# Kernel optimization log

Hardware: AMD Instinct MI355X
Metric: run time of the kernel (lower is better)

## Reference

```python
import jax, jax.numpy as jnp
import numpy as np

G = 256      # num graphs
M = 256      # max nodes per graph
N = G * M    # total nodes
E = N * 16   # total edges
C = 3        # num_class
K = 5        # prototypes per class
D = 128      # embedding_dim
MAXLEN = 3   # max_length


def setup_inputs() -> dict:
    key = jax.random.key(0)
    ks = jax.random.split(key, 8)
    hg = jax.random.normal(ks[0], (G, D), jnp.float32)
    H_init = jax.random.normal(ks[1], (C, K, D), jnp.float32)
    path_weight = jnp.ones((MAXLEN,), jnp.float32) * 0.5
    # per-class edge attention in (0,1), strictly interior for infoloss logs
    sij = jax.random.uniform(ks[2], (C, E), jnp.float32) * 0.98 + 0.01
    # edges constrained within each graph (batch is block-contiguous)
    src = jax.random.randint(ks[3], (E,), 0, N)
    dst = (src // M) * M + jax.random.randint(ks[4], (E,), 0, M)
    edge_index = jnp.stack([src, dst]).astype(jnp.int32)
    batch = (jnp.arange(N) // M).astype(jnp.int32)
    s = jax.random.randint(ks[5], (G,), 0, M).astype(jnp.int32)
    t = jax.random.randint(ks[6], (G,), 0, M).astype(jnp.int32)
    return dict(hg=hg, H_init=H_init, path_weight=path_weight, sij=sij,
                edge_index=edge_index, batch=batch, s=s, t=t)


def check_zero(x):
    return jnp.where(x == 0, x + 1e-8, x)


def to_dense_adj(edge_index, batch, vals):
    # scatter edge vals into [G, M, M] dense per-graph adjacency
    src, dst = edge_index[0], edge_index[1]
    g = batch[src]
    r = src - g * M
    c = dst - g * M
    return jnp.zeros((G, M, M), vals.dtype).at[g, r, c].add(vals)


def infoloss(att):
    r = 0.5
    return (att * jnp.log(att / r + 1e-6)
            + (1 - att) * jnp.log((1 - att) / (1 - r + 1e-6) + 1e-6)).mean()


def path_loss3(Mdj, Adj, s, t, weight):
    gid = jnp.arange(G)
    u = Mdj[gid, s, :]            # [G, M]
    mk = Mdj[gid, :, t]           # [G, M]
    a = Adj[gid, s, :]
    ak = Adj[gid, :, t]
    uk = Mdj[gid, s, t] / check_zero(Adj[gid, s, t])
    for l in range(MAXLEN - 1):
        tmp = (u * mk) / check_zero(a * ak)
        w = jnp.power(tmp.max(axis=1) + 1e-8, jnp.float32(1.0 / (l + 1)))
        uk = uk + weight[l + 1] * w
        # power iteration: u <- u @ Mdj, a <- a @ Adj (batched over graphs)
        u = jnp.einsum('gm,gmn->gn', u, Mdj)
        a = jnp.einsum('gm,gmn->gn', a, Adj)
    uk = uk / MAXLEN
    return -jnp.mean(jnp.log(uk + 1e-8))


def reference(hg, H_init, path_weight, sij, edge_index, batch, s, t):
    # binary dense adjacency (detached in original)
    Adj = jax.lax.stop_gradient(
        to_dense_adj(edge_index, batch, jnp.ones((E,), jnp.float32)))
    weight = jnp.clip(path_weight, 1e-10, 1.0)

    def per_class(Hc, sij_c):
        # per-class prototype attention
        scores = hg @ Hc.T                     # [G, K]
        att = jax.nn.softmax(scores, axis=-1)
        H_emb = att @ Hc                       # [G, D]
        # dense weighted adjacency from per-class edge attention
        Mdj = to_dense_adj(edge_index, batch, sij_c)
        L_path = path_loss3(Mdj, Adj, s, t, weight)
        L_l2 = (jnp.sum(sij_c ** 2) / 2) / G
        L_info = infoloss(sij_c)
        return H_emb, L_info, L_path, L_l2

    H_out, L_info, L_path, L_l2 = jax.vmap(per_class)(H_init, sij)
    return (H_out, L_info.mean(), L_path.mean(), L_l2.mean())
```

## Files before the change

### kernel.cpp

```cpp
#include <hip/hip_runtime.h>
#include <math.h>

#define G 256
#define M 256
#define NNODES (G*M)
#define EDGES (NNODES*16)
#define C 3
#define K 5
#define D 128
#define GM (G*M)

#define OFF_U0   0
#define OFF_MK0  196608
#define OFF_U1   393216
#define OFF_A0   589824
#define OFF_AK0  655360
#define OFF_A1   720896
#define OFF_MST  786432
#define OFF_AST  787200
#define ZERO_FLOATS 787456
#define NB_EDGE  512
#define NB_EMB   384
#define OFF_PINFO 787456
#define OFF_PL2   (OFF_PINFO + NB_EDGE)
#define OFF_PPATH (OFF_PL2 + NB_EDGE)
#define WS_FLOATS (OFF_PPATH + C*G)

__device__ __forceinline__ float waveReduceSum(float v) {
    #pragma unroll
    for (int o = 32; o > 0; o >>= 1) v += __shfl_xor(v, o, 64);
    return v;
}
__device__ __forceinline__ float waveReduceMax(float v) {
    #pragma unroll
    for (int o = 32; o > 0; o >>= 1) v = fmaxf(v, __shfl_xor(v, o, 64));
    return v;
}

__global__ void passA(const float* __restrict__ sij, const int* __restrict__ ei,
                      const int* __restrict__ s, const int* __restrict__ t,
                      const float* __restrict__ hg, const float* __restrict__ Hm,
                      float* __restrict__ out, float* __restrict__ ws) {
    __shared__ int   sS[G], sT[G];
    __shared__ float sc[2][K];
    __shared__ float att[2][K];
    __shared__ float sInfo[4], sL2[4];

    if (blockIdx.x >= NB_EDGE) {
        int half = threadIdx.x >> 7;
        int d = threadIdx.x & 127;
        int pair = (blockIdx.x - NB_EDGE) * 2 + half;
        int c = pair / G, g = pair - c * G;
        float h = hg[g * D + d];
        if (d < K) sc[half][d] = 0.f;
        __syncthreads();
        #pragma unroll
        for (int k = 0; k < K; ++k) {
            float p = h * Hm[(c * K + k) * D + d];
            p = waveReduceSum(p);
            if ((threadIdx.x & 63) == 0) atomicAdd(&sc[half][k], p);
        }
        __syncthreads();
        if (d == 0) {
            float m = sc[half][0];
            #pragma unroll
            for (int k = 1; k < K; ++k) m = fmaxf(m, sc[half][k]);
            float sum = 0.f, ex[K];
            #pragma unroll
            for (int k = 0; k < K; ++k) { ex[k] = __expf(sc[half][k] - m); sum += ex[k]; }
            #pragma unroll
            for (int k = 0; k < K; ++k) att[half][k] = ex[k] / sum;
        }
        __syncthreads();
        float o = 0.f;
        #pragma unroll
        for (int k = 0; k < K; ++k) o += att[half][k] * Hm[(c * K + k) * D + d];
        out[pair * D + d] = o;
        return;
    }

    sS[threadIdx.x] = s[threadIdx.x];
    sT[threadIdx.x] = t[threadIdx.x];
    __syncthreads();

    float* u0  = ws + OFF_U0;
    float* mk0 = ws + OFF_MK0;
    float* a0  = ws + OFF_A0;
    float* ak0 = ws + OFF_AK0;
    float* Mst = ws + OFF_MST;
    float* Ast = ws + OFF_AST;

    int tid = blockIdx.x * 256 + threadIdx.x;
    int e0 = tid * 8;
    int4 srcA = *(const int4*)(ei + e0);
    int4 srcB = *(const int4*)(ei + e0 + 4);
    int4 dstA = *(const int4*)(ei + EDGES + e0);
    int4 dstB = *(const int4*)(ei + EDGES + e0 + 4);
    float4 v0a = *(const float4*)(sij + 0 * EDGES + e0);
    float4 v0b = *(const float4*)(sij + 0 * EDGES + e0 + 4);
    float4 v1a = *(const float4*)(sij + 1 * EDGES + e0);
    float4 v1b = *(const float4*)(sij + 1 * EDGES + e0 + 4);
    float4 v2a = *(const float4*)(sij + 2 * EDGES + e0);
    float4 v2b = *(const float4*)(sij + 2 * EDGES + e0 + 4);

    int srcp[8], dstp[8];
    float vp[3][8];
    *(int4*)&srcp[0] = srcA;  *(int4*)&srcp[4] = srcB;
    *(int4*)&dstp[0] = dstA;  *(int4*)&dstp[4] = dstB;
    *(float4*)&vp[0][0] = v0a; *(float4*)&vp[0][4] = v0b;
    *(float4*)&vp[1][0] = v1a; *(float4*)&vp[1][4] = v1b;
    *(float4*)&vp[2][0] = v2a; *(float4*)&vp[2][4] = v2b;

    float info = 0.f, l2 = 0.f;
    #pragma unroll
    for (int j = 0; j < 8; ++j) {
        int src = srcp[j], dst = dstp[j];
        int g = src >> 8;
        int r = src & 255;
        int c = dst - (g << 8);
        float v[C] = { vp[0][j], vp[1][j], vp[2][j] };
        if (r == sS[g]) {
            #pragma unroll
            for (int cc = 0; cc < C; ++cc) atomicAdd(&u0[cc * GM + (g << 8) + c], v[cc]);
            atomicAdd(&a0[(g << 8) + c], 1.0f);
            if (c == sT[g]) {
                #pragma unroll
                for (int cc = 0; cc < C; ++cc) atomicAdd(&Mst[cc * G + g], v[cc]);
                atomicAdd(&Ast[g], 1.0f);
            }
        }
        if (c == sT[g]) {
            #pragma unroll
            for (int cc = 0; cc < C; ++cc) atomicAdd(&mk0[cc * GM + (g << 8) + r], v[cc]);
            atomicAdd(&ak0[(g << 8) + r], 1.0f);
        }
        #pragma unroll
        for (int cc = 0; cc < C; ++cc) {
            float x = v[cc];
            info += x * __logf(x * 2.0f + 1e-6f)
                  + (1.0f - x) * __logf((1.0f - x) / 0.500001f + 1e-6f);
            l2 += x * x;
        }
    }
    info = waveReduceSum(info);
    l2 = waveReduceSum(l2);
    int wid = threadIdx.x >> 6, lane = threadIdx.x & 63;
    if (lane == 0) { sInfo[wid] = info; sL2[wid] = l2; }
    __syncthreads();
    if (threadIdx.x == 0) {
        float i2 = 0.f, l = 0.f;
        #pragma unroll
        for (int w = 0; w < 4; ++w) { i2 += sInfo[w]; l += sL2[w]; }
        ws[OFF_PINFO + blockIdx.x] = i2;
        ws[OFF_PL2 + blockIdx.x] = l;
    }
}

__global__ void passB(const float* __restrict__ sij, const int* __restrict__ ei,
                      float* __restrict__ ws) {
    const float* u0 = ws + OFF_U0;
    const float* a0 = ws + OFF_A0;
    float* u1 = ws + OFF_U1;
    float* a1 = ws + OFF_A1;

    int tid = blockIdx.x * 256 + threadIdx.x;
    int e0 = tid * 8;
    int4 srcA = *(const int4*)(ei + e0);
    int4 srcB = *(const int4*)(ei + e0 + 4);
    int4 dstA = *(const int4*)(ei + EDGES + e0);
    int4 dstB = *(const int4*)(ei + EDGES + e0 + 4);
    int srcp[8], dstp[8];
    *(int4*)&srcp[0] = srcA;  *(int4*)&srcp[4] = srcB;
    *(int4*)&dstp[0] = dstA;  *(int4*)&dstp[4] = dstB;

    #pragma unroll
    for (int j = 0; j < 8; ++j) {
        int src = srcp[j], dst = dstp[j];
        int g = src >> 8;
        int r = src & 255;
        int c = dst - (g << 8);
        float ar = a0[(g << 8) + r];
        if (ar == 0.0f) continue;
        atomicAdd(&a1[(g << 8) + c], ar);
        int e = e0 + j;
        #pragma unroll
        for (int cc = 0; cc < C; ++cc) {
            float ur = u0[cc * GM + (g << 8) + r];
            atomicAdd(&u1[cc * GM + (g << 8) + c], ur * sij[cc * EDGES + e]);
        }
    }
}

__global__ void pathK(const float* __restrict__ pw, float* __restrict__ ws) {
    int b = blockIdx.x;
    int c = b / G, g = b - c * G;
    int x = threadIdx.x;
    const float* u0  = ws + OFF_U0;
    const float* mk0 = ws + OFF_MK0;
    const float* u1  = ws + OFF_U1;
    const float* a0  = ws + OFF_A0;
    const float* ak0 = ws + OFF_AK0;
    const float* a1  = ws + OFF_A1;

    int gi  = (g << 8) + x;
    int cgi = c * GM + gi;
    float ak = ak0[gi], mk = mk0[cgi];
    float den0 = a0[gi] * ak;  den0 = (den0 == 0.f) ? 1e-8f : den0;
    float t0 = u0[cgi] * mk / den0;
    float den1 = a1[gi] * ak;  den1 = (den1 == 0.f) ? 1e-8f : den1;
    float t1 = u1[cgi] * mk / den1;

    t0 = waveReduceMax(t0);
    t1 = waveReduceMax(t1);
    __shared__ float s0[4], s1[4];
    int wid = x >> 6, lane = x & 63;
    if (lane == 0) { s0[wid] = t0; s1[wid] = t1; }
    __syncthreads();
    if (x == 0) {
        float m0 = s0[0], m1 = s1[0];
        #pragma unroll
        for (int w = 1; w < 4; ++w) { m0 = fmaxf(m0, s0[w]); m1 = fmaxf(m1, s1[w]); }
        float w1 = fminf(fmaxf(pw[1], 1e-10f), 1.0f);
        float w2 = fminf(fmaxf(pw[2], 1e-10f), 1.0f);
        float A = ws[OFF_AST + g];  A = (A == 0.f) ? 1e-8f : A;
        float uk = ws[OFF_MST + c * G + g] / A;
        uk += w1 * (m0 + 1e-8f);
        uk += w2 * sqrtf(m1 + 1e-8f);
        uk *= (1.0f / 3.0f);
        ws[OFF_PPATH + b] = __logf(uk + 1e-8f);
    }
}

__global__ void finalK(const float* __restrict__ ws, float* __restrict__ out) {
    int tid = threadIdx.x;
    float info = 0.f, l2 = 0.f, path = 0.f;
    for (int i = tid; i < NB_EDGE; i += 256) {
        info += ws[OFF_PINFO + i];
        l2   += ws[OFF_PL2 + i];
    }
    for (int i = tid; i < C * G; i += 256) path += ws[OFF_PPATH + i];
    info = waveReduceSum(info);
    l2   = waveReduceSum(l2);
    path = waveReduceSum(path);
    __shared__ float sI[4], sL[4], sP[4];
    int wid = tid >> 6, lane = tid & 63;
    if (lane == 0) { sI[wid] = info; sL[wid] = l2; sP[wid] = path; }
    __syncthreads();
    if (tid == 0) {
        float i2 = 0.f, l = 0.f, p = 0.f;
        #pragma unroll
        for (int w = 0; w < 4; ++w) { i2 += sI[w]; l += sL[w]; p += sP[w]; }
        out[C * G * D + 0] = i2 / (float)(C * EDGES);
        out[C * G * D + 1] = -p / (float)(C * G);
        out[C * G * D + 2] = l / (2.0f * (float)G * (float)C);
    }
}

extern "C" void kernel_launch(void* const* d_in, const int* in_sizes, int n_in,
                              void* d_out, int out_size, void* d_ws, size_t ws_size,
                              hipStream_t stream) {
    const float* hg  = (const float*)d_in[0];
    const float* Hm  = (const float*)d_in[1];
    const float* pw  = (const float*)d_in[2];
    const float* sij = (const float*)d_in[3];
    const int*   ei  = (const int*)d_in[4];
    const int*   s   = (const int*)d_in[6];
    const int*   t   = (const int*)d_in[7];
    float* out = (float*)d_out;
    float* ws  = (float*)d_ws;

    hipMemsetAsync(d_ws, 0, ZERO_FLOATS * sizeof(float), stream);
    passA<<<NB_EDGE + NB_EMB, 256, 0, stream>>>(sij, ei, s, t, hg, Hm, out, ws);
    passB<<<NB_EDGE, 256, 0, stream>>>(sij, ei, ws);
    pathK<<<C * G, M, 0, stream>>>(pw, ws);
    finalK<<<1, 256, 0, stream>>>(ws, out);
}
```

Measured before the change: 42.05 us.

## Replace memset with zeroing kernel, fuse final reduction into path kernel

Replaces the hipMemsetAsync with a custom zeroing kernel that also runs the prototype-embedding work, moving that work out of passA. The final reduction is folded into the path kernel: a global atomic counter lets the last block sum the partials. passB also hoists the a0 gathers into a separate loop so the loads can be issued together. This trims launch count and serial tail latency, at the cost of threadfence/atomic overhead in every path block.

```diff
diff --git a/kernel.cpp b/kernel.cpp
--- a/kernel.cpp
+++ b/kernel.cpp
@@ -18,10 +18,12 @@
 #define OFF_A1   720896
 #define OFF_MST  786432
 #define OFF_AST  787200
-#define ZERO_FLOATS 787456
+#define OFF_CNT  787456
+#define ZERO_FLOATS 787472
 #define NB_EDGE  512
+#define NB_ZERO  512
 #define NB_EMB   384
-#define OFF_PINFO 787456
+#define OFF_PINFO 787472
 #define OFF_PL2   (OFF_PINFO + NB_EDGE)
 #define OFF_PPATH (OFF_PL2 + NB_EDGE)
 #define WS_FLOATS (OFF_PPATH + C*G)
@@ -37,47 +39,57 @@
     return v;
 }
 
+__global__ void zeroEmb(const float* __restrict__ hg, const float* __restrict__ Hm,
+                        float* __restrict__ out, float* __restrict__ ws) {
+    __shared__ float sc[2][K];
+    __shared__ float att[2][K];
+
+    if (blockIdx.x < NB_ZERO) {
+        int tid = blockIdx.x * 256 + threadIdx.x;
+        #pragma unroll
+        for (int it = 0; it < 2; ++it) {
+            int idx = (tid + it * NB_ZERO * 256) * 4;
+            if (idx < ZERO_FLOATS)
+                *(float4*)(ws + idx) = make_float4(0.f, 0.f, 0.f, 0.f);
+        }
+        return;
+    }
+    int half = threadIdx.x >> 7;
+    int d = threadIdx.x & 127;
+    int pair = (blockIdx.x - NB_ZERO) * 2 + half;
+    int c = pair / G, g = pair - c * G;
+    float h = hg[g * D + d];
+    if (d < K) sc[half][d] = 0.f;
+    __syncthreads();
+    #pragma unroll
+    for (int k = 0; k < K; ++k) {
+        float p = h * Hm[(c * K + k) * D + d];
+        p = waveReduceSum(p);
+        if ((threadIdx.x & 63) == 0) atomicAdd(&sc[half][k], p);
+    }
+    __syncthreads();
+    if (d == 0) {
+        float m = sc[half][0];
+        #pragma unroll
+        for (int k = 1; k < K; ++k) m = fmaxf(m, sc[half][k]);
+        float sum = 0.f, ex[K];
+        #pragma unroll
+        for (int k = 0; k < K; ++k) { ex[k] = __expf(sc[half][k] - m); sum += ex[k]; }
+        #pragma unroll
+        for (int k = 0; k < K; ++k) att[half][k] = ex[k] / sum;
+    }
+    __syncthreads();
+    float o = 0.f;
+    #pragma unroll
+    for (int k = 0; k < K; ++k) o += att[half][k] * Hm[(c * K + k) * D + d];
+    out[pair * D + d] = o;
+}
+
 __global__ void passA(const float* __restrict__ sij, const int* __restrict__ ei,
                       const int* __restrict__ s, const int* __restrict__ t,
-                      const float* __restrict__ hg, const float* __restrict__ Hm,
-                      float* __restrict__ out, float* __restrict__ ws) {
+                      float* __restrict__ ws) {
     __shared__ int   sS[G], sT[G];
-    __shared__ float sc[2][K];
-    __shared__ float att[2][K];
     __shared__ float sInfo[4], sL2[4];
-
-    if (blockIdx.x >= NB_EDGE) {
-        int half = threadIdx.x >> 7;
-        int d = threadIdx.x & 127;
-        int pair = (blockIdx.x - NB_EDGE) * 2 + half;
-        int c = pair / G, g = pair - c * G;
-        float h = hg[g * D + d];
-        if (d < K) sc[half][d] = 0.f;
-        __syncthreads();
-        #pragma unroll
-        for (int k = 0; k < K; ++k) {
-            float p = h * Hm[(c * K + k) * D + d];
-            p = waveReduceSum(p);
-            if ((threadIdx.x & 63) == 0) atomicAdd(&sc[half][k], p);
-        }
-        __syncthreads();
-        if (d == 0) {
-            float m = sc[half][0];
-            #pragma unroll
-            for (int k = 1; k < K; ++k) m = fmaxf(m, sc[half][k]);
-            float sum = 0.f, ex[K];
-            #pragma unroll
-            for (int k = 0; k < K; ++k) { ex[k] = __expf(sc[half][k] - m); sum += ex[k]; }
-            #pragma unroll
-            for (int k = 0; k < K; ++k) att[half][k] = ex[k] / sum;
-        }
-        __syncthreads();
-        float o = 0.f;
-        #pragma unroll
-        for (int k = 0; k < K; ++k) o += att[half][k] * Hm[(c * K + k) * D + d];
-        out[pair * D + d] = o;
-        return;
-    }
 
     sS[threadIdx.x] = s[threadIdx.x];
     sT[threadIdx.x] = t[threadIdx.x];
@@ -173,25 +185,30 @@
     *(int4*)&srcp[0] = srcA;  *(int4*)&srcp[4] = srcB;
     *(int4*)&dstp[0] = dstA;  *(int4*)&dstp[4] = dstB;
 
+    int gi[8];
+    float ar[8];
     #pragma unroll
     for (int j = 0; j < 8; ++j) {
-        int src = srcp[j], dst = dstp[j];
-        int g = src >> 8;
-        int r = src & 255;
-        int c = dst - (g << 8);
-        float ar = a0[(g << 8) + r];
-        if (ar == 0.0f) continue;
-        atomicAdd(&a1[(g << 8) + c], ar);
+        gi[j] = (srcp[j] >> 8 << 8);
+        ar[j] = a0[gi[j] + (srcp[j] & 255)];
+    }
+    #pragma unroll
+    for (int j = 0; j < 8; ++j) {
+        if (ar[j] == 0.0f) continue;
+        int r = srcp[j] & 255;
+        int c = dstp[j] - gi[j];
+        atomicAdd(&a1[gi[j] + c], ar[j]);
         int e = e0 + j;
         #pragma unroll
         for (int cc = 0; cc < C; ++cc) {
-            float ur = u0[cc * GM + (g << 8) + r];
-            atomicAdd(&u1[cc * GM + (g << 8) + c], ur * sij[cc * EDGES + e]);
-        }
-    }
-}
-
-__global__ void pathK(const float* __restrict__ pw, float* __restrict__ ws) {
+            float ur = u0[cc * GM + gi[j] + r];
+            atomicAdd(&u1[cc * GM + gi[j] + c], ur * sij[cc * EDGES + e]);
+        }
+    }
+}
+
+__global__ void pathFinal(const float* __restrict__ pw, float* __restrict__ ws,
+                          float* __restrict__ out) {
     int b = blockIdx.x;
     int c = b / G, g = b - c * G;
     int x = threadIdx.x;
@@ -201,6 +218,8 @@
     const float* a0  = ws + OFF_A0;
     const float* ak0 = ws + OFF_AK0;
     const float* a1  = ws + OFF_A1;
+    __shared__ float s0[4], s1[4], s2[4];
+    __shared__ int isLast;
 
     int gi  = (g << 8) + x;
     int cgi = c * GM + gi;
@@ -212,7 +231,6 @@
 
     t0 = waveReduceMax(t0);
     t1 = waveReduceMax(t1);
-    __shared__ float s0[4], s1[4];
     int wid = x >> 6, lane = x & 63;
     if (lane == 0) { s0[wid] = t0; s1[wid] = t1; }
     __syncthreads();
@@ -228,28 +246,29 @@
         uk += w2 * sqrtf(m1 + 1e-8f);
         uk *= (1.0f / 3.0f);
         ws[OFF_PPATH + b] = __logf(uk + 1e-8f);
-    }
-}
-
-__global__ void finalK(const float* __restrict__ ws, float* __restrict__ out) {
-    int tid = threadIdx.x;
+        __threadfence();
+        int done = atomicAdd((int*)(ws + OFF_CNT), 1);
+        isLast = (done == C * G - 1);
+    }
+    __syncthreads();
+    if (!isLast) return;
+    __threadfence();
+
     float info = 0.f, l2 = 0.f, path = 0.f;
-    for (int i = tid; i < NB_EDGE; i += 256) {
+    for (int i = x; i < NB_EDGE; i += 256) {
         info += ws[OFF_PINFO + i];
         l2   += ws[OFF_PL2 + i];
     }
-    for (int i = tid; i < C * G; i += 256) path += ws[OFF_PPATH + i];
+    for (int i = x; i < C * G; i += 256) path += ws[OFF_PPATH + i];
     info = waveReduceSum(info);
     l2   = waveReduceSum(l2);
     path = waveReduceSum(path);
-    __shared__ float sI[4], sL[4], sP[4];
-    int wid = tid >> 6, lane = tid & 63;
-    if (lane == 0) { sI[wid] = info; sL[wid] = l2; sP[wid] = path; }
-    __syncthreads();
-    if (tid == 0) {
+    if (lane == 0) { s0[wid] = info; s1[wid] = l2; s2[wid] = path; }
+    __syncthreads();
+    if (x == 0) {
         float i2 = 0.f, l = 0.f, p = 0.f;
         #pragma unroll
-        for (int w = 0; w < 4; ++w) { i2 += sI[w]; l += sL[w]; p += sP[w]; }
+        for (int w = 0; w < 4; ++w) { i2 += s0[w]; l += s1[w]; p += s2[w]; }
         out[C * G * D + 0] = i2 / (float)(C * EDGES);
         out[C * G * D + 1] = -p / (float)(C * G);
         out[C * G * D + 2] = l / (2.0f * (float)G * (float)C);
@@ -269,9 +288,8 @@
     float* out = (float*)d_out;
     float* ws  = (float*)d_ws;
 
-    hipMemsetAsync(d_ws, 0, ZERO_FLOATS * sizeof(float), stream);
-    passA<<<NB_EDGE + NB_EMB, 256, 0, stream>>>(sij, ei, s, t, hg, Hm, out, ws);
+    zeroEmb<<<NB_ZERO + NB_EMB, 256, 0, stream>>>(hg, Hm, out, ws);
+    passA<<<NB_EDGE, 256, 0, stream>>>(sij, ei, s, t, ws);
     passB<<<NB_EDGE, 256, 0, stream>>>(sij, ei, ws);
-    pathK<<<C * G, M, 0, stream>>>(pw, ws);
-    finalK<<<1, 256, 0, stream>>>(ws, out);
-}
+    pathFinal<<<C * G, M, 0, stream>>>(pw, ws, out);
+}
```

After: 59.54 us. +41.6%, slower.
